# Kernel tuning notes

Measured on AMD Instinct MI355X. Metric: run time of the kernel, lower is better.

Reference implementation:

```python
import jax, jax.numpy as jnp
import numpy as np

DOWNSCALE = 2


def avg_pool2d(x, s):
    b, c, h, w = x.shape
    return x.reshape(b, c, h // s, s, w // s, s).mean(axis=(3, 5))


def upsample_bilinear_align_corners(x, s):
    # matches torch nn.Upsample(scale_factor=s, mode='bilinear', align_corners=True)
    b, c, h, w = x.shape
    H, W = h * s, w * s
    ys = jnp.arange(H, dtype=x.dtype) * ((h - 1) / (H - 1))
    xs = jnp.arange(W, dtype=x.dtype) * ((w - 1) / (W - 1))
    y0 = jnp.floor(ys).astype(jnp.int32)
    y1 = jnp.minimum(y0 + 1, h - 1)
    wy = (ys - y0.astype(x.dtype))[None, None, :, None]
    x0 = jnp.floor(xs).astype(jnp.int32)
    x1 = jnp.minimum(x0 + 1, w - 1)
    wx = (xs - x0.astype(x.dtype))[None, None, None, :]
    rows = x[:, :, y0, :] * (1 - wy) + x[:, :, y1, :] * wy  # [b,c,H,w]
    return rows[:, :, :, x0] * (1 - wx) + rows[:, :, :, x1] * wx  # [b,c,H,W]


def setup_inputs() -> dict:
    key = jax.random.key(0)
    k1, k2, k3, k4, k5, k6 = jax.random.split(key, 6)
    B, INCH, MIDCH, H, W = 8, 64, 32, 128, 128
    primary = jax.random.normal(k1, (B, INCH, H, W), dtype=jnp.float32)
    cross = jax.random.normal(k2, (B, INCH, H, W), dtype=jnp.float32)
    w_theta = jax.random.normal(k3, (MIDCH, INCH), dtype=jnp.float32) / np.sqrt(INCH)
    w_phi = jax.random.normal(k4, (MIDCH, INCH), dtype=jnp.float32) / np.sqrt(INCH)
    w_g = jax.random.normal(k5, (MIDCH, INCH), dtype=jnp.float32) / np.sqrt(INCH)
    w_out = jax.random.normal(k6, (INCH, MIDCH, 3, 3), dtype=jnp.float32) / np.sqrt(MIDCH * 9)
    return {"primary": primary, "cross": cross, "w_theta": w_theta,
            "w_phi": w_phi, "w_g": w_g, "w_out": w_out}


def reference(primary, cross, w_theta, w_phi, w_g, w_out):
    pd = avg_pool2d(primary, DOWNSCALE)  # [b,c,h,w]
    cd = avg_pool2d(cross, DOWNSCALE)
    b, c, h, w = pd.shape
    n = h * w
    pd_flat = pd.reshape(b, c, n)
    cd_flat = cd.reshape(b, c, n)
    # 1x1 convs -> matmuls over channel dim
    g = jnp.einsum('mc,bcn->bnm', w_g, pd_flat)       # [b,n,mid]
    theta = jnp.einsum('mc,bcn->bnm', w_theta, cd_flat)  # queries from cross
    phi = jnp.einsum('mc,bcn->bmn', w_phi, pd_flat)      # keys from primary
    attn = jax.nn.softmax(jnp.einsum('bnm,bmk->bnk', theta, phi), axis=-1)  # [b,n,n]
    y = jnp.einsum('bnk,bkm->bmn', attn, g).reshape(b, -1, h, w)  # [b,mid,h,w]
    y = upsample_bilinear_align_corners(y, DOWNSCALE)
    out = jax.lax.conv_general_dilated(
        y, w_out, window_strides=(1, 1), padding='SAME',
        dimension_numbers=('NCHW', 'OIHW', 'NCHW'))
    return jnp.concatenate((primary, out), axis=1)
```

## Files before the change

### kernel.cpp

```cpp
#include <hip/hip_runtime.h>
#include <math.h>

typedef _Float16 f16;
typedef f16 f16x8 __attribute__((ext_vector_type(8)));
typedef f16 f16x4 __attribute__((ext_vector_type(4)));
typedef __fp16 fp16x2 __attribute__((ext_vector_type(2)));
typedef float f32x4 __attribute__((ext_vector_type(4)));

#define LOG2E 1.44269504088896340736f

__global__ __launch_bounds__(256) void prep_kernel(
    const float* __restrict__ w, const float* __restrict__ w_theta,
    const float* __restrict__ w_phi, const float* __restrict__ w_g,
    f16* __restrict__ wT, float* __restrict__ wTr)
{
    int id = blockIdx.x * 256 + threadIdx.x;
    if (id < 18432) {
        int oc = id / 288, k = id % 288;
        int tap = k >> 5, c = k & 31;
        wT[id] = (f16)w[((size_t)oc * 32 + c) * 9 + tap];
    } else {
        int t2 = id - 18432;
        int tensor = t2 >> 11, idx = t2 & 2047;
        int c = idx >> 5, m = idx & 31;
        const float* src = tensor == 0 ? w_theta : (tensor == 1 ? w_phi : w_g);
        wTr[tensor * 2048 + c * 32 + m] = src[m * 64 + c];
    }
}

__global__ __launch_bounds__(256) void pool_project_kernel(
    const float* __restrict__ primary, const float* __restrict__ cross,
    const float* __restrict__ wTr,
    f16* __restrict__ theta, f16* __restrict__ phi, f16* __restrict__ gP)
{
    __shared__ __align__(16) float pool[2 * 1024];
    __shared__ __align__(16) float wls[3 * 2048];
    int t = threadIdx.x;
    int bx = blockIdx.x;
    int b = bx >> 8, rem = bx & 255;
    int row = rem >> 2, q4 = rem & 3;

#pragma unroll
    for (int i = 0; i < 4; ++i) {
        int chunk = i * 256 + t;
        int xq = chunk & 7;
        int c = (chunk >> 3) & 63, ts = chunk >> 9;
        const float* src = ts ? cross : primary;
        const float* rp = src + (size_t)b * 1048576 + (size_t)c * 16384
                        + (size_t)(2 * row) * 128 + q4 * 32 + xq * 4;
        float4 v0 = *(const float4*)rp;
        float4 v1 = *(const float4*)(rp + 128);
        float2 pv;
        pv.x = 0.25f * ((v0.x + v0.y) + (v1.x + v1.y));
        pv.y = 0.25f * ((v0.z + v0.w) + (v1.z + v1.w));
        *(float2*)&pool[ts * 1024 + c * 16 + 2 * xq] = pv;
    }
#pragma unroll
    for (int i = 0; i < 6; ++i) {
        int cw = i * 256 + t;
        *(float4*)&wls[cw * 4] = *(const float4*)(wTr + cw * 4);
    }
    __syncthreads();

    int mg = t >> 6, lane = t & 63;
    int cg = lane >> 4, px = lane & 15;

    const float* pbaseL = pool + (cg * 16) * 16 + px;
    const float* cbaseL = pbaseL + 1024;
    const float* wlt = wls + (cg * 16) * 32 + mg * 8;
    const float* wlp = wlt + 2048;
    const float* wlg = wlt + 4096;

    float th[8], ph[8], gg[8];
#pragma unroll
    for (int j = 0; j < 8; ++j) { th[j] = 0.f; ph[j] = 0.f; gg[j] = 0.f; }

#pragma unroll
    for (int ci = 0; ci < 16; ++ci) {
        float pdc = pbaseL[ci * 16];
        float cdc = cbaseL[ci * 16];
        float4 a0 = *(const float4*)(wlt + ci * 32);
        float4 a1 = *(const float4*)(wlt + ci * 32 + 4);
        float4 b0 = *(const float4*)(wlp + ci * 32);
        float4 b1 = *(const float4*)(wlp + ci * 32 + 4);
        float4 g0 = *(const float4*)(wlg + ci * 32);
        float4 g1 = *(const float4*)(wlg + ci * 32 + 4);
        th[0] = fmaf(a0.x, cdc, th[0]); th[1] = fmaf(a0.y, cdc, th[1]);
        th[2] = fmaf(a0.z, cdc, th[2]); th[3] = fmaf(a0.w, cdc, th[3]);
        th[4] = fmaf(a1.x, cdc, th[4]); th[5] = fmaf(a1.y, cdc, th[5]);
        th[6] = fmaf(a1.z, cdc, th[6]); th[7] = fmaf(a1.w, cdc, th[7]);
        ph[0] = fmaf(b0.x, pdc, ph[0]); ph[1] = fmaf(b0.y, pdc, ph[1]);
        ph[2] = fmaf(b0.z, pdc, ph[2]); ph[3] = fmaf(b0.w, pdc, ph[3]);
        ph[4] = fmaf(b1.x, pdc, ph[4]); ph[5] = fmaf(b1.y, pdc, ph[5]);
        ph[6] = fmaf(b1.z, pdc, ph[6]); ph[7] = fmaf(b1.w, pdc, ph[7]);
        gg[0] = fmaf(g0.x, pdc, gg[0]); gg[1] = fmaf(g0.y, pdc, gg[1]);
        gg[2] = fmaf(g0.z, pdc, gg[2]); gg[3] = fmaf(g0.w, pdc, gg[3]);
        gg[4] = fmaf(g1.x, pdc, gg[4]); gg[5] = fmaf(g1.y, pdc, gg[5]);
        gg[6] = fmaf(g1.z, pdc, gg[6]); gg[7] = fmaf(g1.w, pdc, gg[7]);
    }

#pragma unroll
    for (int j = 0; j < 8; ++j) {
        th[j] += __shfl_xor(th[j], 16); th[j] += __shfl_xor(th[j], 32);
        ph[j] += __shfl_xor(ph[j], 16); ph[j] += __shfl_xor(ph[j], 32);
        gg[j] += __shfl_xor(gg[j], 16); gg[j] += __shfl_xor(gg[j], 32);
    }

    int n = row * 64 + q4 * 16 + px;
    if (cg == 0) {
        f16x8 tv;
#pragma unroll
        for (int j = 0; j < 8; ++j) tv[j] = (f16)(th[j] * LOG2E);
        *(f16x8*)(theta + ((size_t)b * 4096 + n) * 32 + mg * 8) = tv;
    } else if (cg == 1) {
        f16x8 pv;
#pragma unroll
        for (int j = 0; j < 8; ++j) pv[j] = (f16)ph[j];
        *(f16x8*)(phi + ((size_t)b * 4096 + n) * 32 + mg * 8) = pv;
    } else {
        int w = n & 31, nb32 = n & ~31;
        int d = ((w >> 2) & 3) * 8 + (w >> 4) * 4 + (w & 3);
        int jbase = (cg - 2) * 4;
#pragma unroll
        for (int jj = 0; jj < 4; ++jj) {
            int m = mg * 8 + jbase + jj;
            gP[((size_t)b * 32 + m) * 4096 + nb32 + d] = (f16)gg[jbase + jj];
        }
    }
}

__global__ __launch_bounds__(256) void attn_kernel(
    const f16* __restrict__ theta, const f16* __restrict__ phi,
    const f16* __restrict__ gP, f16* __restrict__ ypart,
    float* __restrict__ lpart)
{
    __shared__ __align__(16) f16 phiS[128 * 40];
    __shared__ __align__(16) f16 gS[32 * 136];
    int t = threadIdx.x;
    int wid = t >> 6, lane = t & 63;
    int g = lane >> 4, c15 = lane & 15;
    int b = blockIdx.y, sp = blockIdx.z;
    int qb = blockIdx.x * 128 + wid * 32;

    f16x8 a_thA = *(const f16x8*)(theta + ((size_t)b * 4096 + qb + c15) * 32 + g * 8);
    f16x8 a_thB = *(const f16x8*)(theta + ((size_t)b * 4096 + qb + 16 + c15) * 32 + g * 8);

    f32x4 YA0 = {0.f, 0.f, 0.f, 0.f}, YA1 = {0.f, 0.f, 0.f, 0.f};
    f32x4 YB0 = {0.f, 0.f, 0.f, 0.f}, YB1 = {0.f, 0.f, 0.f, 0.f};
    float lsumA = 0.f, lsumB = 0.f;
    const f32x4 zinit = {-12.f, -12.f, -12.f, -12.f};

    const f16* phiB = phi + (size_t)b * 4096 * 32;
    const f16* gB   = gP  + (size_t)b * 32 * 4096;

    int i1 = t, i2 = t + 256;
    f16* dp1 = phiS + (i1 >> 2) * 40 + (i1 & 3) * 8;
    f16* dp2 = phiS + (i2 >> 2) * 40 + (i2 & 3) * 8;
    f16* dg1 = gS + (i1 >> 4) * 136 + (i1 & 15) * 8;
    f16* dg2 = gS + (i2 >> 4) * 136 + (i2 & 15) * 8;
    const f16* sp1 = phiB + (size_t)(i1 >> 2) * 32 + (i1 & 3) * 8;
    const f16* sp2 = phiB + (size_t)(i2 >> 2) * 32 + (i2 & 3) * 8;
    const f16* sg1 = gB + (size_t)(i1 >> 4) * 4096 + (i1 & 15) * 8;
    const f16* sg2 = gB + (size_t)(i2 >> 4) * 4096 + (i2 & 15) * 8;

    const int ktbeg = sp * 8, ktend = sp * 8 + 8;

    uint4 r0 = *(const uint4*)(sp1 + (size_t)(ktbeg * 128) * 32);
    uint4 r1 = *(const uint4*)(sp2 + (size_t)(ktbeg * 128) * 32);
    uint4 r2 = *(const uint4*)(sg1 + ktbeg * 128);
    uint4 r3 = *(const uint4*)(sg2 + ktbeg * 128);

    for (int kt = ktbeg; kt < ktend; ++kt) {
        __syncthreads();
        *(uint4*)dp1 = r0;
        *(uint4*)dp2 = r1;
        *(uint4*)dg1 = r2;
        *(uint4*)dg2 = r3;
        if (kt + 1 < ktend) {
            int n1 = (kt + 1) * 128;
            r0 = *(const uint4*)(sp1 + (size_t)n1 * 32);
            r1 = *(const uint4*)(sp2 + (size_t)n1 * 32);
            r2 = *(const uint4*)(sg1 + n1);
            r3 = *(const uint4*)(sg2 + n1);
        }
        __syncthreads();

#pragma unroll
        for (int u = 0; u < 4; ++u) {
            f16x8 bf0 = *(const f16x8*)(phiS + (2 * u * 16 + c15) * 40 + g * 8);
            f16x8 bf1 = *(const f16x8*)(phiS + ((2 * u + 1) * 16 + c15) * 40 + g * 8);
            f16x8 ga0 = *(const f16x8*)(gS + c15 * 136 + u * 32 + g * 8);
            f16x8 ga1 = *(const f16x8*)(gS + (16 + c15) * 136 + u * 32 + g * 8);

            f32x4 s0A = __builtin_amdgcn_mfma_f32_16x16x32_f16(bf0, a_thA, zinit, 0, 0, 0);
            f32x4 s1A = __builtin_amdgcn_mfma_f32_16x16x32_f16(bf1, a_thA, zinit, 0, 0, 0);
            f32x4 s0B = __builtin_amdgcn_mfma_f32_16x16x32_f16(bf0, a_thB, zinit, 0, 0, 0);
            f32x4 s1B = __builtin_amdgcn_mfma_f32_16x16x32_f16(bf1, a_thB, zinit, 0, 0, 0);

            union { unsigned int u4[4]; f16x8 v; } pbA, pbB;
#pragma unroll
            for (int half = 0; half < 2; ++half) {
                f32x4 sv = half ? s1A : s0A;
                float p0 = __builtin_amdgcn_exp2f(sv[0]);
                float p1 = __builtin_amdgcn_exp2f(sv[1]);
                float p2 = __builtin_amdgcn_exp2f(sv[2]);
                float p3 = __builtin_amdgcn_exp2f(sv[3]);
                lsumA += (p0 + p1) + (p2 + p3);
                union { fp16x2 v; unsigned int u; } ca, cb;
                ca.v = __builtin_amdgcn_cvt_pkrtz(p0, p1);
                cb.v = __builtin_amdgcn_cvt_pkrtz(p2, p3);
                pbA.u4[half * 2 + 0] = ca.u;
                pbA.u4[half * 2 + 1] = cb.u;
            }
#pragma unroll
            for (int half = 0; half < 2; ++half) {
                f32x4 sv = half ? s1B : s0B;
                float p0 = __builtin_amdgcn_exp2f(sv[0]);
                float p1 = __builtin_amdgcn_exp2f(sv[1]);
                float p2 = __builtin_amdgcn_exp2f(sv[2]);
                float p3 = __builtin_amdgcn_exp2f(sv[3]);
                lsumB += (p0 + p1) + (p2 + p3);
                union { fp16x2 v; unsigned int u; } ca, cb;
                ca.v = __builtin_amdgcn_cvt_pkrtz(p0, p1);
                cb.v = __builtin_amdgcn_cvt_pkrtz(p2, p3);
                pbB.u4[half * 2 + 0] = ca.u;
                pbB.u4[half * 2 + 1] = cb.u;
            }
            YA0 = __builtin_amdgcn_mfma_f32_16x16x32_f16(ga0, pbA.v, YA0, 0, 0, 0);
            YA1 = __builtin_amdgcn_mfma_f32_16x16x32_f16(ga1, pbA.v, YA1, 0, 0, 0);
            YB0 = __builtin_amdgcn_mfma_f32_16x16x32_f16(ga0, pbB.v, YB0, 0, 0, 0);
            YB1 = __builtin_amdgcn_mfma_f32_16x16x32_f16(ga1, pbB.v, YB1, 0, 0, 0);
        }
    }

    lsumA += __shfl_xor(lsumA, 16);
    lsumA += __shfl_xor(lsumA, 32);
    lsumB += __shfl_xor(lsumB, 16);
    lsumB += __shfl_xor(lsumB, 32);
    if (g == 0) {
        lpart[((size_t)(sp * 8 + b)) * 4096 + qb + c15] = lsumA;
        lpart[((size_t)(sp * 8 + b)) * 4096 + qb + 16 + c15] = lsumB;
    }

    f16* yp = ypart + ((size_t)(sp * 8 + b) * 32) * 4096 + qb;
#pragma unroll
    for (int r = 0; r < 4; ++r) {
        yp[(size_t)(g * 4 + r) * 4096 + c15]           = (f16)YA0[r];
        yp[(size_t)(16 + g * 4 + r) * 4096 + c15]      = (f16)YA1[r];
        yp[(size_t)(g * 4 + r) * 4096 + 16 + c15]      = (f16)YB0[r];
        yp[(size_t)(16 + g * 4 + r) * 4096 + 16 + c15] = (f16)YB1[r];
    }
}

__global__ __launch_bounds__(256) void combine_kernel(
    const f16* __restrict__ ypart, const float* __restrict__ lpart,
    float* __restrict__ y)
{
    int gid = blockIdx.x * 256 + threadIdx.x;
    int n4 = (gid & 1023) * 4;
    int bm = gid >> 10;
    int b = bm >> 5, m = bm & 31;
    float acc0 = 0.f, acc1 = 0.f, acc2 = 0.f, acc3 = 0.f;
    float l0 = 0.f, l1 = 0.f, l2 = 0.f, l3 = 0.f;
#pragma unroll
    for (int s = 0; s < 4; ++s) {
        f16x4 yv = *(const f16x4*)(ypart + ((size_t)(s * 8 + b) * 32 + m) * 4096 + n4);
        float4 lv = *(const float4*)(lpart + ((size_t)(s * 8 + b)) * 4096 + n4);
        acc0 += (float)yv[0]; acc1 += (float)yv[1];
        acc2 += (float)yv[2]; acc3 += (float)yv[3];
        l0 += lv.x; l1 += lv.y; l2 += lv.z; l3 += lv.w;
    }
    float4 o = make_float4(acc0 / l0, acc1 / l1, acc2 / l2, acc3 / l3);
    *(float4*)(y + (size_t)bm * 4096 + n4) = o;
}

__global__ __launch_bounds__(256) void upsample_kernel(
    const float* __restrict__ y, f16* __restrict__ yup)
{
    int gid = blockIdx.x * 256 + threadIdx.x;
    int xi = gid & 63, Y = (gid >> 6) & 127, bc = gid >> 13;
    const float r = 63.0f / 127.0f;
    float fy = (float)Y * r;
    int y0 = (int)fy; int y1 = min(y0 + 1, 63);
    float wy = fy - (float)y0;
    const float* r0 = y + (size_t)bc * 4096 + y0 * 64;
    const float* r1 = y + (size_t)bc * 4096 + y1 * 64;
    union { unsigned int u; f16 h[2]; } pk;
#pragma unroll
    for (int k = 0; k < 2; ++k) {
        int X = 2 * xi + k;
        float fx = (float)X * r;
        int x0 = (int)fx; int x1 = min(x0 + 1, 63);
        float wx = fx - (float)x0;
        float a  = r0[x0] * (1.f - wy) + r1[x0] * wy;
        float bb = r0[x1] * (1.f - wy) + r1[x1] * wy;
        pk.h[k] = (f16)(a * (1.f - wx) + bb * wx);
    }
    *(unsigned int*)&yup[((size_t)bc * 128 + Y) * 128 + 2 * xi] = pk.u;
}

__global__ __launch_bounds__(256) void conv3x3_kernel(
    const f16* __restrict__ yup, const f16* __restrict__ wT,
    float* __restrict__ out)
{
    __shared__ f16 tile[32 * 4 * 132];
    int tY = blockIdx.x, b = blockIdx.y;
    int t = threadIdx.x;

    {
        int u = t & 127, c = u >> 2, rr = u & 3;
        int s0 = c * 528 + rr * 132 + ((t < 128) ? 0 : 130);
        *(unsigned int*)&tile[s0] = 0u;
    }
#pragma unroll
    for (int rd = 0; rd < 8; ++rd) {
        int id = rd * 256 + t;
        int c = id >> 6, rr = (id >> 4) & 3, seg = id & 15;
        int iy = 2 * tY - 1 + rr;
        uint4 v = make_uint4(0u, 0u, 0u, 0u);
        if ((unsigned)iy < 128u)
            v = *(const uint4*)(yup + (((size_t)b * 32 + c) * 128 + iy) * 128 + seg * 8);
        int base = c * 528 + rr * 132 + 2 + seg * 8;
        *(unsigned int*)&tile[base + 0] = v.x;
        *(unsigned int*)&tile[base + 2] = v.y;
        *(unsigned int*)&tile[base + 4] = v.z;
        *(unsigned int*)&tile[base + 6] = v.w;
    }
    __syncthreads();

    int wid = t >> 6, lane = t & 63, g = lane >> 4, c15 = lane & 15;
    f32x4 acc[4][4];
#pragma unroll
    for (int mt = 0; mt < 4; ++mt)
#pragma unroll
        for (int nt = 0; nt < 4; ++nt) acc[mt][nt] = (f32x4){0.f, 0.f, 0.f, 0.f};

#pragma unroll
    for (int tap = 0; tap < 9; ++tap) {
        const int dy = tap / 3, dx = tap % 3;
        f16x8 a0 = *(const f16x8*)(wT + (size_t)(c15) * 288 + tap * 32 + g * 8);
        f16x8 a1 = *(const f16x8*)(wT + (size_t)(16 + c15) * 288 + tap * 32 + g * 8);
        f16x8 a2 = *(const f16x8*)(wT + (size_t)(32 + c15) * 288 + tap * 32 + g * 8);
        f16x8 a3 = *(const f16x8*)(wT + (size_t)(48 + c15) * 288 + tap * 32 + g * 8);
#pragma unroll
        for (int nt = 0; nt < 4; ++nt) {
            int ntg = wid * 4 + nt;
            int r_out = ntg >> 3, x0 = (ntg & 7) * 16;
            int base = (g * 8) * 528 + (r_out + dy) * 132 + 1 + x0 + c15 + dx;
            f16x8 bf;
#pragma unroll
            for (int j = 0; j < 8; ++j) bf[j] = tile[base + j * 528];
            acc[0][nt] = __builtin_amdgcn_mfma_f32_16x16x32_f16(a0, bf, acc[0][nt], 0, 0, 0);
            acc[1][nt] = __builtin_amdgcn_mfma_f32_16x16x32_f16(a1, bf, acc[1][nt], 0, 0, 0);
            acc[2][nt] = __builtin_amdgcn_mfma_f32_16x16x32_f16(a2, bf, acc[2][nt], 0, 0, 0);
            acc[3][nt] = __builtin_amdgcn_mfma_f32_16x16x32_f16(a3, bf, acc[3][nt], 0, 0, 0);
        }
    }

#pragma unroll
    for (int mt = 0; mt < 4; ++mt)
#pragma unroll
        for (int nt = 0; nt < 4; ++nt) {
            int ntg = wid * 4 + nt;
            int r_out = ntg >> 3, x0 = (ntg & 7) * 16;
            float* ob = out + ((size_t)b * 128 + 64 + mt * 16 + g * 4) * 16384
                            + (2 * tY + r_out) * 128 + x0 + c15;
#pragma unroll
            for (int r = 0; r < 4; ++r)
                ob[(size_t)r * 16384] = acc[mt][nt][r];
        }
}

__global__ __launch_bounds__(256) void copy_primary_kernel(
    const float4* __restrict__ p, float4* __restrict__ out)
{
    int gid = blockIdx.x * 256 + threadIdx.x;
    const int chunk = (64 * 16384) / 4;
    int b = gid >> 18;
    int off = gid & (chunk - 1);
    out[(size_t)b * 2 * chunk + off] = p[gid];
}

extern "C" void kernel_launch(void* const* d_in, const int* in_sizes, int n_in,
                              void* d_out, int out_size, void* d_ws, size_t ws_size,
                              hipStream_t stream)
{
    const float* primary = (const float*)d_in[0];
    const float* cross   = (const float*)d_in[1];
    const float* w_theta = (const float*)d_in[2];
    const float* w_phi   = (const float*)d_in[3];
    const float* w_g     = (const float*)d_in[4];
    const float* w_out   = (const float*)d_in[5];
    float* out = (float*)d_out;

    char* wsb = (char*)d_ws;
    f16*   wT    = (f16*)(wsb);
    float* wTr   = (float*)(wsb + 36864);
    f16*   theta = (f16*)(wsb + (1u << 16));
    f16*   phi   = (f16*)(wsb + (1u << 16) + (2u << 20));
    f16*   gP    = (f16*)(wsb + (1u << 16) + (4u << 20));
    float* y     = (float*)(wsb + (1u << 16) + (6u << 20));
    f16*   yup   = (f16*)(wsb + (1u << 16) + (10u << 20));
    f16*   ypart = (f16*)(wsb + (1u << 16) + (18u << 20));
    float* lpart = (float*)(wsb + (1u << 16) + (26u << 20));

    prep_kernel<<<96, 256, 0, stream>>>(w_out, w_theta, w_phi, w_g, wT, wTr);
    pool_project_kernel<<<2048, 256, 0, stream>>>(primary, cross, wTr,
                                                  theta, phi, gP);
    attn_kernel<<<dim3(32, 8, 4), 256, 0, stream>>>(theta, phi, gP, ypart, lpart);
    combine_kernel<<<1024, 256, 0, stream>>>(ypart, lpart, y);
    upsample_kernel<<<8192, 256, 0, stream>>>(y, yup);
    conv3x3_kernel<<<dim3(64, 8), 256, 0, stream>>>(yup, wT, out);
    copy_primary_kernel<<<8192, 256, 0, stream>>>((const float4*)primary, (float4*)out);
}
```

Before: 92.59 us.

## Fuse primary copy into attention kernel and merge combine with upsample

The passthrough copy of primary into the output is moved into the tail of the attention kernel, so each attention block also copies 2048 float4s. This removes a separate launch and lets the memory-bound copy overlap with compute-bound attention. The split-K combine and the bilinear upsample are merged into one kernel that keeps the combined 64x64 map in shared memory, which removes the fp32 y round trip through global memory and one more launch. In exchange the fused upsample runs only 256 blocks doing serial per-thread loops, and the attention tail gains extra memory traffic.

```diff
diff --git a/kernel.cpp b/kernel.cpp
--- a/kernel.cpp
+++ b/kernel.cpp
@@ -132,7 +132,8 @@
 __global__ __launch_bounds__(256) void attn_kernel(
     const f16* __restrict__ theta, const f16* __restrict__ phi,
     const f16* __restrict__ gP, f16* __restrict__ ypart,
-    float* __restrict__ lpart)
+    float* __restrict__ lpart,
+    const float4* __restrict__ prim4, float4* __restrict__ out4)
 {
     __shared__ __align__(16) f16 phiS[128 * 40];
     __shared__ __align__(16) f16 gS[32 * 136];
@@ -250,53 +251,75 @@
         yp[(size_t)(g * 4 + r) * 4096 + 16 + c15]      = (f16)YB0[r];
         yp[(size_t)(16 + g * 4 + r) * 4096 + 16 + c15] = (f16)YB1[r];
     }
-}
-
-__global__ __launch_bounds__(256) void combine_kernel(
+
+    int blk = (blockIdx.z * 8 + blockIdx.y) * 32 + blockIdx.x;
+#pragma unroll
+    for (int i = 0; i < 8; ++i) {
+        int idx = blk * 2048 + i * 256 + t;
+        int bs = idx >> 18;
+        int off = idx & 262143;
+        out4[(size_t)bs * 524288 + off] = prim4[idx];
+    }
+}
+
+__global__ __launch_bounds__(256) void comb_upsample_kernel(
     const f16* __restrict__ ypart, const float* __restrict__ lpart,
-    float* __restrict__ y)
-{
-    int gid = blockIdx.x * 256 + threadIdx.x;
-    int n4 = (gid & 1023) * 4;
-    int bm = gid >> 10;
-    int b = bm >> 5, m = bm & 31;
-    float acc0 = 0.f, acc1 = 0.f, acc2 = 0.f, acc3 = 0.f;
-    float l0 = 0.f, l1 = 0.f, l2 = 0.f, l3 = 0.f;
+    f16* __restrict__ yup)
+{
+    __shared__ float yl[4096];
+    int t = threadIdx.x;
+    int b = blockIdx.x >> 5, m = blockIdx.x & 31;
+
+    int n0 = t * 16;
+    float acc[16], ls[16];
+#pragma unroll
+    for (int j = 0; j < 16; ++j) { acc[j] = 0.f; ls[j] = 0.f; }
 #pragma unroll
     for (int s = 0; s < 4; ++s) {
-        f16x4 yv = *(const f16x4*)(ypart + ((size_t)(s * 8 + b) * 32 + m) * 4096 + n4);
-        float4 lv = *(const float4*)(lpart + ((size_t)(s * 8 + b)) * 4096 + n4);
-        acc0 += (float)yv[0]; acc1 += (float)yv[1];
-        acc2 += (float)yv[2]; acc3 += (float)yv[3];
-        l0 += lv.x; l1 += lv.y; l2 += lv.z; l3 += lv.w;
-    }
-    float4 o = make_float4(acc0 / l0, acc1 / l1, acc2 / l2, acc3 / l3);
-    *(float4*)(y + (size_t)bm * 4096 + n4) = o;
-}
-
-__global__ __launch_bounds__(256) void upsample_kernel(
-    const float* __restrict__ y, f16* __restrict__ yup)
-{
-    int gid = blockIdx.x * 256 + threadIdx.x;
-    int xi = gid & 63, Y = (gid >> 6) & 127, bc = gid >> 13;
+        const f16* yb = ypart + ((size_t)(s * 8 + b) * 32 + m) * 4096 + n0;
+        const float* lb = lpart + (size_t)(s * 8 + b) * 4096 + n0;
+        f16x8 v0 = *(const f16x8*)yb;
+        f16x8 v1 = *(const f16x8*)(yb + 8);
+#pragma unroll
+        for (int j = 0; j < 8; ++j) {
+            acc[j] += (float)v0[j];
+            acc[8 + j] += (float)v1[j];
+        }
+#pragma unroll
+        for (int j4 = 0; j4 < 4; ++j4) {
+            float4 lv = *(const float4*)(lb + j4 * 4);
+            ls[j4 * 4 + 0] += lv.x; ls[j4 * 4 + 1] += lv.y;
+            ls[j4 * 4 + 2] += lv.z; ls[j4 * 4 + 3] += lv.w;
+        }
+    }
+#pragma unroll
+    for (int j = 0; j < 16; ++j) yl[n0 + j] = acc[j] / ls[j];
+    __syncthreads();
+
     const float r = 63.0f / 127.0f;
+    int Y = t >> 1, xbase = (t & 1) * 32;
     float fy = (float)Y * r;
     int y0 = (int)fy; int y1 = min(y0 + 1, 63);
     float wy = fy - (float)y0;
-    const float* r0 = y + (size_t)bc * 4096 + y0 * 64;
-    const float* r1 = y + (size_t)bc * 4096 + y1 * 64;
-    union { unsigned int u; f16 h[2]; } pk;
-#pragma unroll
-    for (int k = 0; k < 2; ++k) {
-        int X = 2 * xi + k;
-        float fx = (float)X * r;
-        int x0 = (int)fx; int x1 = min(x0 + 1, 63);
-        float wx = fx - (float)x0;
-        float a  = r0[x0] * (1.f - wy) + r1[x0] * wy;
-        float bb = r0[x1] * (1.f - wy) + r1[x1] * wy;
-        pk.h[k] = (f16)(a * (1.f - wx) + bb * wx);
-    }
-    *(unsigned int*)&yup[((size_t)bc * 128 + Y) * 128 + 2 * xi] = pk.u;
+    const float* r0 = yl + y0 * 64;
+    const float* r1 = yl + y1 * 64;
+    f16* orow = yup + ((size_t)(b * 32 + m) * 128 + Y) * 128;
+#pragma unroll 8
+    for (int j = 0; j < 32; ++j) {
+        int xi = xbase + j;
+        union { unsigned int u; f16 h[2]; } pk;
+#pragma unroll
+        for (int k = 0; k < 2; ++k) {
+            int X = 2 * xi + k;
+            float fx = (float)X * r;
+            int x0 = (int)fx; int x1 = min(x0 + 1, 63);
+            float wx = fx - (float)x0;
+            float a  = r0[x0] * (1.f - wy) + r1[x0] * wy;
+            float bb = r0[x1] * (1.f - wy) + r1[x1] * wy;
+            pk.h[k] = (f16)(a * (1.f - wx) + bb * wx);
+        }
+        *(unsigned int*)&orow[2 * xi] = pk.u;
+    }
 }
 
 __global__ __launch_bounds__(256) void conv3x3_kernel(
@@ -371,16 +394,6 @@
         }
 }
 
-__global__ __launch_bounds__(256) void copy_primary_kernel(
-    const float4* __restrict__ p, float4* __restrict__ out)
-{
-    int gid = blockIdx.x * 256 + threadIdx.x;
-    const int chunk = (64 * 16384) / 4;
-    int b = gid >> 18;
-    int off = gid & (chunk - 1);
-    out[(size_t)b * 2 * chunk + off] = p[gid];
-}
-
 extern "C" void kernel_launch(void* const* d_in, const int* in_sizes, int n_in,
                               void* d_out, int out_size, void* d_ws, size_t ws_size,
                               hipStream_t stream)
@@ -399,7 +412,6 @@
     f16*   theta = (f16*)(wsb + (1u << 16));
     f16*   phi   = (f16*)(wsb + (1u << 16) + (2u << 20));
     f16*   gP    = (f16*)(wsb + (1u << 16) + (4u << 20));
-    float* y     = (float*)(wsb + (1u << 16) + (6u << 20));
     f16*   yup   = (f16*)(wsb + (1u << 16) + (10u << 20));
     f16*   ypart = (f16*)(wsb + (1u << 16) + (18u << 20));
     float* lpart = (float*)(wsb + (1u << 16) + (26u << 20));
@@ -407,9 +419,9 @@
     prep_kernel<<<96, 256, 0, stream>>>(w_out, w_theta, w_phi, w_g, wT, wTr);
     pool_project_kernel<<<2048, 256, 0, stream>>>(primary, cross, wTr,
                                                   theta, phi, gP);
-    attn_kernel<<<dim3(32, 8, 4), 256, 0, stream>>>(theta, phi, gP, ypart, lpart);
-    combine_kernel<<<1024, 256, 0, stream>>>(ypart, lpart, y);
-    upsample_kernel<<<8192, 256, 0, stream>>>(y, yup);
+    attn_kernel<<<dim3(32, 8, 4), 256, 0, stream>>>(theta, phi, gP, ypart, lpart,
+                                                    (const float4*)primary,
+                                                    (float4*)out);
+    comb_upsample_kernel<<<256, 256, 0, stream>>>(ypart, lpart, yup);
     conv3x3_kernel<<<dim3(64, 8), 256, 0, stream>>>(yup, wT, out);
-    copy_primary_kernel<<<8192, 256, 0, stream>>>((const float4*)primary, (float4*)out);
-}
+}
```

Result: slower. 107.2 us (+15.8%).
